# Performance work log

Measured on AMD Instinct MI355X. Metric: run time of the kernel, lower is better.

The kernel has to match this reference:

```python
import jax, jax.numpy as jnp
import numpy as np

T, N, E, D_IN, D_OUT = 8, 50000, 800000, 64, 64


def setup_inputs() -> dict:
    key = jax.random.key(0)
    k = jax.random.split(key, 7)
    x = jax.random.normal(k[0], (T, N, D_IN), dtype=jnp.float32)
    edge_index = jax.random.randint(k[1], (2, E), 0, N, dtype=jnp.int32)
    edge_time = jax.random.uniform(k[2], (E,), dtype=jnp.float32)
    node_time = jnp.sort(jax.random.uniform(k[3], (T,), dtype=jnp.float32))
    edge_weight = jax.random.uniform(k[4], (E,), dtype=jnp.float32)
    W = jax.random.normal(k[5], (D_IN, D_OUT), dtype=jnp.float32) / jnp.sqrt(jnp.float32(D_IN))
    b = jnp.zeros((D_OUT,), dtype=jnp.float32)
    return {"x": x, "edge_index": edge_index, "edge_time": edge_time,
            "node_time": node_time, "edge_weight": edge_weight, "W": W, "b": b}


def reference(x, edge_index, edge_time, node_time, edge_weight, W, b):
    # Faithful translation of DGN.forward: per-timestep temporal GNN conv.
    # DGNConv (assumed canonical form): edges with edge_time <= node_time[i]
    # are active; messages x[src]*edge_weight are sum-scattered to dst, then a
    # Linear(in, out) is applied. lax.scan replaces the Python time loop.
    src, dst = edge_index[0], edge_index[1]

    def step(_, xt_t):
        xt, t = xt_t  # xt: [N, D_IN], t: scalar
        w = jnp.where(edge_time <= t, edge_weight, jnp.float32(0.0))  # [E]
        msg = xt[src] * w[:, None]                                    # [E, D_IN]
        agg = jax.ops.segment_sum(msg, dst, num_segments=N)           # [N, D_IN]
        return None, agg @ W + b                                      # [N, D_OUT]

    _, out = jax.lax.scan(step, None, (x, node_time))
    return out  # [T, N, D_OUT]
```

## Files before the change

kernel.cpp:

```cpp
#include <hip/hip_runtime.h>
#include <cstdint>
#include <cstddef>

#define TSTEPS 8
#define D 64

static __device__ __forceinline__ unsigned short f2bf(float f) {
    unsigned int u = __float_as_uint(f);
    return (unsigned short)((u + 0x7FFFu + ((u >> 16) & 1u)) >> 16);
}
static __device__ __forceinline__ float bf2f(unsigned short h) {
    return __uint_as_float(((unsigned int)h) << 16);
}

__global__ __launch_bounds__(256) void hist_kernel(
    const int* __restrict__ dst, const float* __restrict__ etime,
    const float* __restrict__ ntime, int E,
    int* __restrict__ cnt, unsigned int* __restrict__ keyA,
    unsigned int* __restrict__ rankA)
{
    int e = blockIdx.x * 256 + threadIdx.x;
    if (e >= E) return;
    float et = etime[e];
    int t0 = 0;
#pragma unroll
    for (int t = 0; t < TSTEPS; t++) t0 += (ntime[t] < et) ? 1 : 0;
    if (t0 < TSTEPS) {
        unsigned int key = ((unsigned int)dst[e] << 3) | (unsigned int)t0;
        unsigned int r = (unsigned int)atomicAdd(&cnt[key], 1);
        keyA[e] = key;
        rankA[e] = r;
    } else {
        keyA[e] = 0xFFFFFFFFu;
    }
}

__global__ __launch_bounds__(256) void reduce_kernel(const int* __restrict__ cnt,
                                                     int* __restrict__ sums, int n) {
    __shared__ int red[256];
    int tid = threadIdx.x;
    int base = blockIdx.x * 1024 + tid * 4;
    int tot = 0;
#pragma unroll
    for (int j = 0; j < 4; j++) { int i = base + j; tot += (i < n) ? cnt[i] : 0; }
    red[tid] = tot;
    __syncthreads();
    for (int s = 128; s > 0; s >>= 1) {
        if (tid < s) red[tid] += red[tid + s];
        __syncthreads();
    }
    if (tid == 0) sums[blockIdx.x] = red[0];
}

__global__ __launch_bounds__(256) void scanwrite_kernel(const int* __restrict__ cnt,
                                                        const int* __restrict__ sums,
                                                        int* __restrict__ rowptr, int n) {
    __shared__ int buf[256];
    int tid = threadIdx.x;
    int base = blockIdx.x * 1024 + tid * 4;
    int v[4];
    int tot = 0;
#pragma unroll
    for (int j = 0; j < 4; j++) { int i = base + j; v[j] = (i < n) ? cnt[i] : 0; tot += v[j]; }

    buf[tid] = tot;
    __syncthreads();
    for (int off = 1; off < 256; off <<= 1) {
        int t = (tid >= off) ? buf[tid - off] : 0;
        __syncthreads();
        buf[tid] += t;
        __syncthreads();
    }
    int exclThread = buf[tid] - tot;

    int bp = 0;
    for (int j = 0; j < blockIdx.x; j++) bp += sums[j];

    int running = bp + exclThread;
#pragma unroll
    for (int j = 0; j < 4; j++) {
        int i = base + j;
        if (i < n) { rowptr[i] = running; running += v[j]; }
    }
    if (blockIdx.x == (int)gridDim.x - 1 && tid == 255) rowptr[n] = running;
}

__global__ __launch_bounds__(256) void bucket_kernel(
    const int* __restrict__ src, const float* __restrict__ ew, int E,
    const unsigned int* __restrict__ keyA, const unsigned int* __restrict__ rankA,
    const int* __restrict__ rowptr, uint2* __restrict__ meta)
{
    int e = blockIdx.x * 256 + threadIdx.x;
    if (e >= E) return;
    unsigned int key = keyA[e];
    if (key == 0xFFFFFFFFu) return;
    int p = rowptr[key] + (int)rankA[e];
    uint2 m;
    m.x = (unsigned int)src[e];
    m.y = __float_as_uint(ew[e]);
    meta[p] = m;
}

__global__ __launch_bounds__(256) void cvt_kernel(const float* __restrict__ x,
                                                  unsigned short* __restrict__ xb,
                                                  long n4) {
    long i = (long)blockIdx.x * blockDim.x + threadIdx.x;
    if (i >= n4) return;
    float4 v = ((const float4*)x)[i];
    ushort4 u;
    u.x = f2bf(v.x); u.y = f2bf(v.y); u.z = f2bf(v.z); u.w = f2bf(v.w);
    ((ushort4*)xb)[i] = u;
}

template<bool USE_BF16>
__global__ __launch_bounds__(256) void fused_gather_kernel(
    const float* __restrict__ xf, const unsigned short* __restrict__ xb,
    const uint2* __restrict__ meta, const int* __restrict__ rowptr,
    const float* __restrict__ W, const float* __restrict__ b,
    float* __restrict__ out, int N)
{
    __shared__ float Wlds[64 * 64];
    __shared__ float aggS[4][TSTEPS][64];

    int tid = threadIdx.x;
#pragma unroll
    for (int i = 0; i < 16; i++) Wlds[tid + i * 256] = W[tid + i * 256];
    __syncthreads();

    int wslot = tid >> 6;
    int lane  = tid & 63;
    int g = lane >> 4;
    int q = lane & 15;
    int n = blockIdx.x * 4 + wslot;

    const size_t plane = (size_t)N * D;

    float4 acc[TSTEPS];
#pragma unroll
    for (int t = 0; t < TSTEPS; t++) acc[t] = make_float4(0.f, 0.f, 0.f, 0.f);

    if (n < N) {
        int rbase = n * 8;
        int base = rowptr[rbase];
#pragma unroll
        for (int t = 0; t < TSTEPS; t++) {
            int end = rowptr[rbase + t + 1];
            if (USE_BF16) {
                const unsigned short* xp = xb + (size_t)t * plane + q * 4;
                for (int p = base; p < end; p += 8) {
                    int i0 = p + g, i1 = p + g + 4;
                    if (i0 < end) {
                        uint2 m = meta[i0];
                        float w = __uint_as_float(m.y);
                        ushort4 u = *reinterpret_cast<const ushort4*>(xp + ((size_t)m.x << 6));
                        acc[t].x = fmaf(bf2f(u.x), w, acc[t].x);
                        acc[t].y = fmaf(bf2f(u.y), w, acc[t].y);
                        acc[t].z = fmaf(bf2f(u.z), w, acc[t].z);
                        acc[t].w = fmaf(bf2f(u.w), w, acc[t].w);
                    }
                    if (i1 < end) {
                        uint2 m = meta[i1];
                        float w = __uint_as_float(m.y);
                        ushort4 u = *reinterpret_cast<const ushort4*>(xp + ((size_t)m.x << 6));
                        acc[t].x = fmaf(bf2f(u.x), w, acc[t].x);
                        acc[t].y = fmaf(bf2f(u.y), w, acc[t].y);
                        acc[t].z = fmaf(bf2f(u.z), w, acc[t].z);
                        acc[t].w = fmaf(bf2f(u.w), w, acc[t].w);
                    }
                }
            } else {
                const float4* xp = reinterpret_cast<const float4*>(xf + (size_t)t * plane) + q;
                for (int p = base; p < end; p += 8) {
                    int i0 = p + g, i1 = p + g + 4;
                    if (i0 < end) {
                        uint2 m = meta[i0];
                        float w = __uint_as_float(m.y);
                        float4 v = xp[(size_t)m.x << 4];
                        acc[t].x = fmaf(v.x, w, acc[t].x);
                        acc[t].y = fmaf(v.y, w, acc[t].y);
                        acc[t].z = fmaf(v.z, w, acc[t].z);
                        acc[t].w = fmaf(v.w, w, acc[t].w);
                    }
                    if (i1 < end) {
                        uint2 m = meta[i1];
                        float w = __uint_as_float(m.y);
                        float4 v = xp[(size_t)m.x << 4];
                        acc[t].x = fmaf(v.x, w, acc[t].x);
                        acc[t].y = fmaf(v.y, w, acc[t].y);
                        acc[t].z = fmaf(v.z, w, acc[t].z);
                        acc[t].w = fmaf(v.w, w, acc[t].w);
                    }
                }
            }
        }
    }

#pragma unroll
    for (int t = 0; t < TSTEPS; t++) {
        acc[t].x += __shfl_xor(acc[t].x, 16); acc[t].y += __shfl_xor(acc[t].y, 16);
        acc[t].z += __shfl_xor(acc[t].z, 16); acc[t].w += __shfl_xor(acc[t].w, 16);
        acc[t].x += __shfl_xor(acc[t].x, 32); acc[t].y += __shfl_xor(acc[t].y, 32);
        acc[t].z += __shfl_xor(acc[t].z, 32); acc[t].w += __shfl_xor(acc[t].w, 32);
    }

    if (lane < 16) {
#pragma unroll
        for (int t = 0; t < TSTEPS; t++)
            *reinterpret_cast<float4*>(&aggS[wslot][t][lane * 4]) = acc[t];
    }
    __syncthreads();

    float o[TSTEPS];
    float bias = b[lane];
#pragma unroll
    for (int t = 0; t < TSTEPS; t++) o[t] = bias;

    for (int kc = 0; kc < 16; kc++) {
        float w0 = Wlds[(4 * kc + 0) * 64 + lane];
        float w1 = Wlds[(4 * kc + 1) * 64 + lane];
        float w2 = Wlds[(4 * kc + 2) * 64 + lane];
        float w3 = Wlds[(4 * kc + 3) * 64 + lane];
#pragma unroll
        for (int t = 0; t < TSTEPS; t++) {
            float4 a = *reinterpret_cast<const float4*>(&aggS[wslot][t][4 * kc]);
            o[t] = fmaf(a.x, w0, fmaf(a.y, w1, fmaf(a.z, w2, fmaf(a.w, w3, o[t]))));
        }
    }

    if (n < N) {
        size_t ob = (size_t)n * D + lane;
#pragma unroll
        for (int t = 0; t < TSTEPS; t++) out[(size_t)t * plane + ob] = o[t];
    }
}

extern "C" void kernel_launch(void* const* d_in, const int* in_sizes, int n_in,
                              void* d_out, int out_size, void* d_ws, size_t ws_size,
                              hipStream_t stream)
{
    const float* x     = (const float*)d_in[0];
    const int*   eidx  = (const int*)d_in[1];
    const float* etime = (const float*)d_in[2];
    const float* ntime = (const float*)d_in[3];
    const float* ew    = (const float*)d_in[4];
    const float* W     = (const float*)d_in[5];
    const float* b     = (const float*)d_in[6];
    float* out = (float*)d_out;

    const int T = in_sizes[3];
    const int E = in_sizes[1] / 2;
    const int N = in_sizes[0] / (T * D);
    const int N8 = N * 8;

    const int* src = eidx;
    const int* dst = eidx + E;

    int nb = (N8 + 1023) / 1024;

    char* base = (char*)d_ws;
    uint2* meta   = (uint2*)base;
    int*   cnt    = (int*)(base + 8ll * E);
    int*   rowptr = cnt + N8;
    int*   sums   = rowptr + N8 + 1;
    size_t offK = 8ll * E + 4ll * (2ll * N8 + 1 + nb);
    offK = (offK + 15) & ~(size_t)15;
    unsigned int* keyA  = (unsigned int*)(base + offK);
    unsigned int* rankA = keyA + E;
    unsigned short* xb  = (unsigned short*)(base + offK);

    size_t xbBytes = 2ll * T * N * D;
    size_t krBytes = 8ll * E;
    size_t needB = offK + (xbBytes > krBytes ? xbBytes : krBytes);
    bool useBf16 = (ws_size >= needB);

    hipMemsetAsync(cnt, 0, (size_t)N8 * sizeof(int), stream);

    hist_kernel<<<(E + 255) / 256, 256, 0, stream>>>(dst, etime, ntime, E,
                                                     cnt, keyA, rankA);
    reduce_kernel<<<nb, 256, 0, stream>>>(cnt, sums, N8);
    scanwrite_kernel<<<nb, 256, 0, stream>>>(cnt, sums, rowptr, N8);
    bucket_kernel<<<(E + 255) / 256, 256, 0, stream>>>(src, ew, E, keyA, rankA,
                                                       rowptr, meta);

    if (useBf16) {
        long n4 = (long)T * N * D / 4;
        cvt_kernel<<<(int)((n4 + 255) / 256), 256, 0, stream>>>(x, xb, n4);
        fused_gather_kernel<true><<<(N + 3) / 4, 256, 0, stream>>>(
            x, xb, meta, rowptr, W, b, out, N);
    } else {
        fused_gather_kernel<false><<<(N + 3) / 4, 256, 0, stream>>>(
            x, xb, meta, rowptr, W, b, out, N);
    }
}
```

Baseline: 515.7 us.

## Bucket edges per node and gather all timesteps per edge with node-major bf16 x

Edges are now bucketed only by destination node, not by (node, first-active-timestep). Each edge's first active step is packed into the low 3 bits of the source index. The gather reads one meta entry per edge and accumulates its contribution into every timestep from t0 onward. The bf16 copy of x is transposed to a node-major [N][T][D] layout so the up to 8 timestep reads per edge fall in one contiguous 1 KB row. The bf16 conversion is also fused into the histogram launch, and the rank array shrinks to 16-bit. This cuts meta traffic and improves locality of the x gathers. In exchange, rank counters are truncated to 16 bits and the bucket kernel recomputes t0.

```diff
diff --git a/kernel.cpp b/kernel.cpp
--- a/kernel.cpp
+++ b/kernel.cpp
@@ -13,25 +13,37 @@
     return __uint_as_float(((unsigned int)h) << 16);
 }
 
-__global__ __launch_bounds__(256) void hist_kernel(
+__global__ __launch_bounds__(256) void prep_kernel(
+    const float* __restrict__ x, unsigned short* __restrict__ xb,
     const int* __restrict__ dst, const float* __restrict__ etime,
-    const float* __restrict__ ntime, int E,
-    int* __restrict__ cnt, unsigned int* __restrict__ keyA,
-    unsigned int* __restrict__ rankA)
+    const float* __restrict__ ntime,
+    int* __restrict__ cnt, unsigned short* __restrict__ rankA,
+    int E, int N, int histBlocks, int blocksPerPlane)
 {
-    int e = blockIdx.x * 256 + threadIdx.x;
-    if (e >= E) return;
-    float et = etime[e];
-    int t0 = 0;
-#pragma unroll
-    for (int t = 0; t < TSTEPS; t++) t0 += (ntime[t] < et) ? 1 : 0;
-    if (t0 < TSTEPS) {
-        unsigned int key = ((unsigned int)dst[e] << 3) | (unsigned int)t0;
-        unsigned int r = (unsigned int)atomicAdd(&cnt[key], 1);
-        keyA[e] = key;
-        rankA[e] = r;
+    int tid = threadIdx.x;
+    if ((int)blockIdx.x < histBlocks) {
+        int e = blockIdx.x * 256 + tid;
+        if (e < E) {
+            float et = etime[e];
+            int t0 = 0;
+#pragma unroll
+            for (int t = 0; t < TSTEPS; t++) t0 += (ntime[t] < et) ? 1 : 0;
+            if (t0 < TSTEPS)
+                rankA[e] = (unsigned short)atomicAdd(&cnt[dst[e]], 1);
+        }
     } else {
-        keyA[e] = 0xFFFFFFFFu;
+        int bb = blockIdx.x - histBlocks;
+        int t  = bb / blocksPerPlane;
+        int r  = bb - t * blocksPerPlane;
+        int j  = r * 256 + tid;
+        int d4 = j & 15;
+        int n  = j >> 4;
+        if (n < N) {
+            float4 v = ((const float4*)x)[((size_t)t * N + n) * 16 + d4];
+            ushort4 u;
+            u.x = f2bf(v.x); u.y = f2bf(v.y); u.z = f2bf(v.z); u.w = f2bf(v.w);
+            ((ushort4*)xb)[(size_t)n * 128 + t * 16 + d4] = u;
+        }
     }
 }
 
@@ -86,30 +98,24 @@
 }
 
 __global__ __launch_bounds__(256) void bucket_kernel(
-    const int* __restrict__ src, const float* __restrict__ ew, int E,
-    const unsigned int* __restrict__ keyA, const unsigned int* __restrict__ rankA,
-    const int* __restrict__ rowptr, uint2* __restrict__ meta)
+    const int* __restrict__ src, const int* __restrict__ dst,
+    const float* __restrict__ etime, const float* __restrict__ ew,
+    const float* __restrict__ ntime, int E,
+    const unsigned short* __restrict__ rankA, const int* __restrict__ rowptr,
+    uint2* __restrict__ meta)
 {
     int e = blockIdx.x * 256 + threadIdx.x;
     if (e >= E) return;
-    unsigned int key = keyA[e];
-    if (key == 0xFFFFFFFFu) return;
-    int p = rowptr[key] + (int)rankA[e];
+    float et = etime[e];
+    int t0 = 0;
+#pragma unroll
+    for (int t = 0; t < TSTEPS; t++) t0 += (ntime[t] < et) ? 1 : 0;
+    if (t0 >= TSTEPS) return;
+    int p = rowptr[dst[e]] + (int)rankA[e];
     uint2 m;
-    m.x = (unsigned int)src[e];
+    m.x = ((unsigned int)src[e] << 3) | (unsigned int)t0;
     m.y = __float_as_uint(ew[e]);
     meta[p] = m;
-}
-
-__global__ __launch_bounds__(256) void cvt_kernel(const float* __restrict__ x,
-                                                  unsigned short* __restrict__ xb,
-                                                  long n4) {
-    long i = (long)blockIdx.x * blockDim.x + threadIdx.x;
-    if (i >= n4) return;
-    float4 v = ((const float4*)x)[i];
-    ushort4 u;
-    u.x = f2bf(v.x); u.y = f2bf(v.y); u.z = f2bf(v.z); u.w = f2bf(v.w);
-    ((ushort4*)xb)[i] = u;
 }
 
 template<bool USE_BF16>
@@ -140,55 +146,75 @@
     for (int t = 0; t < TSTEPS; t++) acc[t] = make_float4(0.f, 0.f, 0.f, 0.f);
 
     if (n < N) {
-        int rbase = n * 8;
-        int base = rowptr[rbase];
-#pragma unroll
-        for (int t = 0; t < TSTEPS; t++) {
-            int end = rowptr[rbase + t + 1];
+        int p0 = rowptr[n], p1 = rowptr[n + 1];
+        for (int p = p0; p < p1; p += 8) {
+            int i0 = p + g, i1 = p + g + 4;
             if (USE_BF16) {
-                const unsigned short* xp = xb + (size_t)t * plane + q * 4;
-                for (int p = base; p < end; p += 8) {
-                    int i0 = p + g, i1 = p + g + 4;
-                    if (i0 < end) {
-                        uint2 m = meta[i0];
-                        float w = __uint_as_float(m.y);
-                        ushort4 u = *reinterpret_cast<const ushort4*>(xp + ((size_t)m.x << 6));
-                        acc[t].x = fmaf(bf2f(u.x), w, acc[t].x);
-                        acc[t].y = fmaf(bf2f(u.y), w, acc[t].y);
-                        acc[t].z = fmaf(bf2f(u.z), w, acc[t].z);
-                        acc[t].w = fmaf(bf2f(u.w), w, acc[t].w);
+                if (i0 < p1) {
+                    uint2 m = meta[i0];
+                    int t0 = (int)(m.x & 7u);
+                    float w = __uint_as_float(m.y);
+                    const unsigned short* xp = xb + ((size_t)(m.x >> 3) << 9) + (q << 2);
+#pragma unroll
+                    for (int t = 0; t < TSTEPS; t++) {
+                        if (t >= t0) {
+                            ushort4 u = *reinterpret_cast<const ushort4*>(xp + (t << 6));
+                            acc[t].x = fmaf(bf2f(u.x), w, acc[t].x);
+                            acc[t].y = fmaf(bf2f(u.y), w, acc[t].y);
+                            acc[t].z = fmaf(bf2f(u.z), w, acc[t].z);
+                            acc[t].w = fmaf(bf2f(u.w), w, acc[t].w);
+                        }
                     }
-                    if (i1 < end) {
-                        uint2 m = meta[i1];
-                        float w = __uint_as_float(m.y);
-                        ushort4 u = *reinterpret_cast<const ushort4*>(xp + ((size_t)m.x << 6));
-                        acc[t].x = fmaf(bf2f(u.x), w, acc[t].x);
-                        acc[t].y = fmaf(bf2f(u.y), w, acc[t].y);
-                        acc[t].z = fmaf(bf2f(u.z), w, acc[t].z);
-                        acc[t].w = fmaf(bf2f(u.w), w, acc[t].w);
+                }
+                if (i1 < p1) {
+                    uint2 m = meta[i1];
+                    int t0 = (int)(m.x & 7u);
+                    float w = __uint_as_float(m.y);
+                    const unsigned short* xp = xb + ((size_t)(m.x >> 3) << 9) + (q << 2);
+#pragma unroll
+                    for (int t = 0; t < TSTEPS; t++) {
+                        if (t >= t0) {
+                            ushort4 u = *reinterpret_cast<const ushort4*>(xp + (t << 6));
+                            acc[t].x = fmaf(bf2f(u.x), w, acc[t].x);
+                            acc[t].y = fmaf(bf2f(u.y), w, acc[t].y);
+                            acc[t].z = fmaf(bf2f(u.z), w, acc[t].z);
+                            acc[t].w = fmaf(bf2f(u.w), w, acc[t].w);
+                        }
                     }
                 }
             } else {
-                const float4* xp = reinterpret_cast<const float4*>(xf + (size_t)t * plane) + q;
-                for (int p = base; p < end; p += 8) {
-                    int i0 = p + g, i1 = p + g + 4;
-                    if (i0 < end) {
-                        uint2 m = meta[i0];
-                        float w = __uint_as_float(m.y);
-                        float4 v = xp[(size_t)m.x << 4];
-                        acc[t].x = fmaf(v.x, w, acc[t].x);
-                        acc[t].y = fmaf(v.y, w, acc[t].y);
-                        acc[t].z = fmaf(v.z, w, acc[t].z);
-                        acc[t].w = fmaf(v.w, w, acc[t].w);
+                if (i0 < p1) {
+                    uint2 m = meta[i0];
+                    int t0 = (int)(m.x & 7u);
+                    float w = __uint_as_float(m.y);
+                    const float4* xp = reinterpret_cast<const float4*>(
+                        xf + (size_t)(m.x >> 3) * D) + q;
+#pragma unroll
+                    for (int t = 0; t < TSTEPS; t++) {
+                        if (t >= t0) {
+                            float4 v = xp[(size_t)t * (plane >> 2)];
+                            acc[t].x = fmaf(v.x, w, acc[t].x);
+                            acc[t].y = fmaf(v.y, w, acc[t].y);
+                            acc[t].z = fmaf(v.z, w, acc[t].z);
+                            acc[t].w = fmaf(v.w, w, acc[t].w);
+                        }
                     }
-                    if (i1 < end) {
-                        uint2 m = meta[i1];
-                        float w = __uint_as_float(m.y);
-                        float4 v = xp[(size_t)m.x << 4];
-                        acc[t].x = fmaf(v.x, w, acc[t].x);
-                        acc[t].y = fmaf(v.y, w, acc[t].y);
-                        acc[t].z = fmaf(v.z, w, acc[t].z);
-                        acc[t].w = fmaf(v.w, w, acc[t].w);
+                }
+                if (i1 < p1) {
+                    uint2 m = meta[i1];
+                    int t0 = (int)(m.x & 7u);
+                    float w = __uint_as_float(m.y);
+                    const float4* xp = reinterpret_cast<const float4*>(
+                        xf + (size_t)(m.x >> 3) * D) + q;
+#pragma unroll
+                    for (int t = 0; t < TSTEPS; t++) {
+                        if (t >= t0) {
+                            float4 v = xp[(size_t)t * (plane >> 2)];
+                            acc[t].x = fmaf(v.x, w, acc[t].x);
+                            acc[t].y = fmaf(v.y, w, acc[t].y);
+                            acc[t].z = fmaf(v.z, w, acc[t].z);
+                            acc[t].w = fmaf(v.w, w, acc[t].w);
+                        }
                     }
                 }
             }
@@ -250,41 +276,39 @@
     const int T = in_sizes[3];
     const int E = in_sizes[1] / 2;
     const int N = in_sizes[0] / (T * D);
-    const int N8 = N * 8;
 
     const int* src = eidx;
     const int* dst = eidx + E;
 
-    int nb = (N8 + 1023) / 1024;
+    int nb = (N + 1023) / 1024;
 
     char* base = (char*)d_ws;
     uint2* meta   = (uint2*)base;
     int*   cnt    = (int*)(base + 8ll * E);
-    int*   rowptr = cnt + N8;
-    int*   sums   = rowptr + N8 + 1;
-    size_t offK = 8ll * E + 4ll * (2ll * N8 + 1 + nb);
-    offK = (offK + 15) & ~(size_t)15;
-    unsigned int* keyA  = (unsigned int*)(base + offK);
-    unsigned int* rankA = keyA + E;
-    unsigned short* xb  = (unsigned short*)(base + offK);
-
-    size_t xbBytes = 2ll * T * N * D;
-    size_t krBytes = 8ll * E;
-    size_t needB = offK + (xbBytes > krBytes ? xbBytes : krBytes);
+    int*   rowptr = cnt + N;
+    int*   sums   = rowptr + N + 1;
+    unsigned short* rankA = (unsigned short*)(sums + nb);
+    size_t offX = 8ll * E + 4ll * (2ll * N + 1 + nb) + 2ll * E;
+    offX = (offX + 15) & ~(size_t)15;
+    unsigned short* xb = (unsigned short*)(base + offX);
+    size_t needB = offX + 2ll * (size_t)T * N * D;
     bool useBf16 = (ws_size >= needB);
 
-    hipMemsetAsync(cnt, 0, (size_t)N8 * sizeof(int), stream);
-
-    hist_kernel<<<(E + 255) / 256, 256, 0, stream>>>(dst, etime, ntime, E,
-                                                     cnt, keyA, rankA);
-    reduce_kernel<<<nb, 256, 0, stream>>>(cnt, sums, N8);
-    scanwrite_kernel<<<nb, 256, 0, stream>>>(cnt, sums, rowptr, N8);
-    bucket_kernel<<<(E + 255) / 256, 256, 0, stream>>>(src, ew, E, keyA, rankA,
-                                                       rowptr, meta);
+    hipMemsetAsync(cnt, 0, (size_t)N * sizeof(int), stream);
+
+    int histBlocks = (E + 255) / 256;
+    int blocksPerPlane = (16 * N + 255) / 256;
+    int prepGrid = useBf16 ? (histBlocks + T * blocksPerPlane) : histBlocks;
+
+    prep_kernel<<<prepGrid, 256, 0, stream>>>(x, xb, dst, etime, ntime,
+                                              cnt, rankA, E, N, histBlocks,
+                                              blocksPerPlane);
+    reduce_kernel<<<nb, 256, 0, stream>>>(cnt, sums, N);
+    scanwrite_kernel<<<nb, 256, 0, stream>>>(cnt, sums, rowptr, N);
+    bucket_kernel<<<histBlocks, 256, 0, stream>>>(src, dst, etime, ew, ntime, E,
+                                                  rankA, rowptr, meta);
 
     if (useBf16) {
-        long n4 = (long)T * N * D / 4;
-        cvt_kernel<<<(int)((n4 + 255) / 256), 256, 0, stream>>>(x, xb, n4);
         fused_gather_kernel<true><<<(N + 3) / 4, 256, 0, stream>>>(
             x, xb, meta, rowptr, W, b, out, N);
     } else {
```

Measured after the change: 466.9 us. 9.5% less time.
